# Optimization experiments

Measured on AMD Instinct MI355X. Metric: run time of the kernel, lower is better.

The kernel has to match this reference:

```python
import jax, jax.numpy as jnp
import numpy as np

N, E, F0, HEADS, B, OUT = 100000, 1600000, 128, 4, 64, 32
CHANNELS = [16, 8, 4, 2]
NEG_SLOPE = 0.2


def setup_inputs() -> dict:
    key = jax.random.key(0)
    ks = jax.random.split(key, 40)
    inp = {}
    inp['x'] = jax.random.normal(ks[0], (N, F0), dtype=jnp.float32)
    inp['edge_index'] = jax.random.randint(ks[1], (2, E), 0, N, dtype=jnp.int64)
    inp['batch'] = jnp.sort(jax.random.randint(ks[2], (N,), 0, B, dtype=jnp.int64))
    # GATConv params per layer: W [in, heads*out], att_src/att_dst [heads, out], bias [heads*out]
    in_dim = F0
    ki = 3
    for li, oc in enumerate(CHANNELS, start=1):
        scale = 1.0 / np.sqrt(in_dim)
        inp[f'W{li}'] = jax.random.normal(ks[ki], (in_dim, HEADS * oc), dtype=jnp.float32) * scale
        inp[f'a_src{li}'] = jax.random.normal(ks[ki + 1], (HEADS, oc), dtype=jnp.float32) * 0.1
        inp[f'a_dst{li}'] = jax.random.normal(ks[ki + 2], (HEADS, oc), dtype=jnp.float32) * 0.1
        inp[f'b{li}'] = jnp.zeros((HEADS * oc,), dtype=jnp.float32)
        ki += 3
        in_dim = HEADS * oc
    inp['W_fc'] = jax.random.normal(ks[ki], (2 * HEADS, OUT), dtype=jnp.float32) * (1.0 / np.sqrt(2 * HEADS))
    inp['b_fc'] = jnp.zeros((OUT,), dtype=jnp.float32)
    return inp


def gat_layer(x, src, dst, W, a_src, a_dst, b, oc):
    n = x.shape[0]
    h = (x @ W).reshape(n, HEADS, oc)                    # [N, H, C]
    al_s = jnp.einsum('nhc,hc->nh', h, a_src)            # [N, H]
    al_d = jnp.einsum('nhc,hc->nh', h, a_dst)
    e = jax.nn.leaky_relu(al_s[src] + al_d[dst], NEG_SLOPE)  # [E, H]
    # segment softmax over incoming edges per destination node
    m = jax.ops.segment_max(e, dst, num_segments=n)
    m = jnp.where(jnp.isfinite(m), m, 0.0)
    ex = jnp.exp(e - m[dst])
    s = jax.ops.segment_sum(ex, dst, num_segments=n)
    alpha = ex / (s[dst] + 1e-16)                        # [E, H]
    out = jax.ops.segment_sum(h[src] * alpha[:, :, None], dst, num_segments=n)
    return out.reshape(n, HEADS * oc) + b


def reference(x, edge_index, batch, W1, a_src1, a_dst1, b1, W2, a_src2, a_dst2, b2,
              W3, a_src3, a_dst3, b3, W4, a_src4, a_dst4, b4, W_fc, b_fc):
    n = x.shape[0]
    loops = jnp.arange(n, dtype=edge_index.dtype)
    src = jnp.concatenate([edge_index[0], loops])   # PyG GATConv adds self-loops
    dst = jnp.concatenate([edge_index[1], loops])
    params = [(W1, a_src1, a_dst1, b1), (W2, a_src2, a_dst2, b2),
              (W3, a_src3, a_dst3, b3), (W4, a_src4, a_dst4, b4)]
    h = x
    for (W, a_s, a_d, b), oc in zip(params, CHANNELS):
        h = jax.nn.relu(gat_layer(h, src, dst, W, a_s, a_d, b, oc))
        # dropout(0.3) is identity at inference
    # global mean pool over graphs in the batch
    sums = jax.ops.segment_sum(h, batch, num_segments=B)
    cnt = jax.ops.segment_sum(jnp.ones((n,), h.dtype), batch, num_segments=B)
    pooled = sums / jnp.maximum(cnt, 1.0)[:, None]
    return pooled @ W_fc + b_fc
```

## Files before the change

kernel.cpp:

```cpp
#include <hip/hip_runtime.h>
#include <hip/hip_bf16.h>

#define NNODES 100000
#define NEDGES 1600000
#define NHEADS 4
#define NGRAPH 64
#define NOUTF  32
#define BSH    9
#define NBUK   ((NNODES + 511) >> 9)
#define BPAD   16
#define BCAP   9216
#define CGRID  512
#define G1GRID ((NNODES + 63) / 64)

__device__ __forceinline__ unsigned short f2bf(float f) {
    union { float f; unsigned u; } v;
    v.f = f;
    unsigned r = v.u + 0x7FFF + ((v.u >> 16) & 1);
    return (unsigned short)(r >> 16);
}
__device__ __forceinline__ float bflo(unsigned u) {
    union { unsigned u; float f; } v;
    v.u = u << 16;
    return v.f;
}
__device__ __forceinline__ float bfhi(unsigned u) {
    union { unsigned u; float f; } v;
    v.u = u & 0xFFFF0000u;
    return v.f;
}

__device__ __forceinline__ bool ei_is_int64(const int* __restrict__ ei) {
    int acc = 0;
    #pragma unroll
    for (int i = 0; i < 32; i++) acc |= ei[2 * i + 1];
    return acc == 0;
}

__device__ __forceinline__ void fma4(float4& a, float s, const float4& b) {
    a.x += s * b.x;
    a.y += s * b.y;
    a.z += s * b.z;
    a.w += s * b.w;
}

__global__ __launch_bounds__(256) void gat_coarse_gemm1_kernel(
        const int* __restrict__ ei, const int* __restrict__ bt,
        int* __restrict__ bkcur, int* __restrict__ packed, int* __restrict__ bat,
        const float* __restrict__ x, const float* __restrict__ W1,
        const float* __restrict__ as1, const float* __restrict__ ad1,
        unsigned short* __restrict__ h1, float* __restrict__ al_s,
        float* __restrict__ al_d, int ne, int n) {
    __shared__ float smem[64 * 64 + 64 * 132];
    const int tid = threadIdx.x;
    if (blockIdx.x < CGRID) {
        int* hist = (int*)smem;
        int* base = hist + NBUK;
        for (int i = tid; i < NBUK; i += 256) hist[i] = 0;
        __syncthreads();
        bool wide = ei_is_int64(ei);
        int chunk = (ne + CGRID - 1) / CGRID;
        int e0 = blockIdx.x * chunk;
        int e1 = min(e0 + chunk, ne);
        for (int i = e0 + tid; i < e1; i += 256) {
            int d = wide ? ei[2 * (ne + i)] : ei[ne + i];
            atomicAdd(&hist[d >> BSH], 1);
        }
        __syncthreads();
        for (int i = tid; i < NBUK; i += 256)
            base[i] = hist[i] ? atomicAdd(&bkcur[i * BPAD], hist[i]) : 0;
        __syncthreads();
        for (int i = tid; i < NBUK; i += 256) hist[i] = 0;
        __syncthreads();
        for (int i = e0 + tid; i < e1; i += 256) {
            int s = wide ? ei[2 * i] : ei[i];
            int d = wide ? ei[2 * (ne + i)] : ei[ne + i];
            int bk = d >> BSH;
            int pos = base[bk] + atomicAdd(&hist[bk], 1);
            if (pos < BCAP) packed[bk * BCAP + pos] = s | ((d & 511) << 17);
        }
        int gid = blockIdx.x * 256 + tid;
        for (int i = gid; i < n; i += CGRID * 256) bat[i] = wide ? bt[2 * i] : bt[i];
    } else {
        constexpr int DIN = 128, DOUT = 64, KTILE = 64;
        constexpr int OG = DOUT / 4;
        constexpr int NPB = 64;
        constexpr int S = DIN + 4;
        constexpr int C = DOUT / NHEADS;
        float* Wl = smem;
        float* xs = smem + KTILE * DOUT;
        const int base = (blockIdx.x - CGRID) * NPB;
        constexpr int KC = DIN / 4;
        for (int i = tid; i < NPB * KC; i += 256) {
            int nn = i / KC, kc = i - nn * KC;
            int nd = base + nn;
            float4 v = (nd < n) ? ((const float4*)x)[(size_t)nd * KC + kc]
                                : make_float4(0.f, 0.f, 0.f, 0.f);
            *(float4*)&xs[nn * S + kc * 4] = v;
        }
        const int og = tid % OG;
        const int ng = tid / OG;
        const int n0 = ng * 4;
        float4 acc[4] = {};
        for (int kt = 0; kt < DIN; kt += KTILE) {
            __syncthreads();
            for (int i = tid; i < KTILE * OG; i += 256)
                ((float4*)Wl)[i] = ((const float4*)W1)[kt * OG + i];
            __syncthreads();
            #pragma unroll 2
            for (int k = 0; k < KTILE; k += 4) {
                float4 wv[4], xv[4];
                #pragma unroll
                for (int j = 0; j < 4; j++)
                    wv[j] = *(const float4*)&Wl[(k + j) * DOUT + og * 4];
                #pragma unroll
                for (int r = 0; r < 4; r++)
                    xv[r] = *(const float4*)&xs[(n0 + r) * S + kt + k];
                #pragma unroll
                for (int r = 0; r < 4; r++) {
                    fma4(acc[r], xv[r].x, wv[0]);
                    fma4(acc[r], xv[r].y, wv[1]);
                    fma4(acc[r], xv[r].z, wv[2]);
                    fma4(acc[r], xv[r].w, wv[3]);
                }
            }
        }
        float4 asv = ((const float4*)as1)[og];
        float4 adv = ((const float4*)ad1)[og];
        #pragma unroll
        for (int r = 0; r < 4; r++) {
            int node = base + n0 + r;
            bool ok = node < n;
            if (ok) {
                ushort4 o;
                o.x = f2bf(acc[r].x);
                o.y = f2bf(acc[r].y);
                o.z = f2bf(acc[r].z);
                o.w = f2bf(acc[r].w);
                ((ushort4*)h1)[(size_t)node * OG + og] = o;
            }
            float ps = acc[r].x * asv.x + acc[r].y * asv.y + acc[r].z * asv.z + acc[r].w * asv.w;
            float pd = acc[r].x * adv.x + acc[r].y * adv.y + acc[r].z * adv.z + acc[r].w * adv.w;
            #pragma unroll
            for (int off = 1; off < C / 4; off <<= 1) {
                ps += __shfl_xor(ps, off);
                pd += __shfl_xor(pd, off);
            }
            if (ok && (og % (C / 4)) == 0) {
                int hh = og / (C / 4);
                al_s[node * NHEADS + hh] = ps;
                al_d[node * NHEADS + hh] = pd;
            }
        }
    }
}

__global__ __launch_bounds__(1024) void gat_fine_kernel(
        const int* __restrict__ packed, const int* __restrict__ bkcur,
        int* __restrict__ row_ptr, int* __restrict__ col, int n) {
    __shared__ int bscan[256];
    __shared__ int dg[512];
    __shared__ int excl[512];
    __shared__ int partial[256];
    __shared__ int cur[512];
    int b = blockIdx.x;
    int tid = threadIdx.x;
    if (tid < 256) bscan[tid] = (tid < NBUK) ? bkcur[tid * BPAD] : 0;
    if (tid < 512) dg[tid] = 0;
    __syncthreads();
    for (int off = 1; off < 256; off <<= 1) {
        int u = (tid < 256 && tid >= off) ? bscan[tid - off] : 0;
        __syncthreads();
        if (tid < 256) bscan[tid] += u;
        __syncthreads();
    }
    int cntb = bkcur[b * BPAD];
    int csr0 = bscan[b] - cntb;
    int pbeg = b * BCAP;
    int pend = pbeg + cntb;
    for (int t = pbeg + tid; t < pend; t += 1024)
        atomicAdd(&dg[packed[t] >> 17], 1);
    __syncthreads();
    int a0 = 0, a1 = 0, s = 0;
    if (tid < 256) {
        a0 = dg[2 * tid];
        a1 = dg[2 * tid + 1];
        s = a0 + a1;
        partial[tid] = s;
    }
    __syncthreads();
    for (int off = 1; off < 256; off <<= 1) {
        int u = (tid < 256 && tid >= off) ? partial[tid - off] : 0;
        __syncthreads();
        if (tid < 256) partial[tid] += u;
        __syncthreads();
    }
    if (tid < 256) {
        int ebase = partial[tid] - s;
        excl[2 * tid] = ebase;
        excl[2 * tid + 1] = ebase + a0;
        cur[2 * tid] = ebase;
        cur[2 * tid + 1] = ebase + a0;
    }
    __syncthreads();
    int node0 = b << BSH;
    if (tid < 512) {
        int nd = node0 + tid;
        if (nd < n) row_ptr[nd] = csr0 + excl[tid];
    }
    if (b == NBUK - 1 && tid == 0) row_ptr[n] = bscan[NBUK - 1];
    for (int t = pbeg + tid; t < pend; t += 1024) {
        int v = packed[t];
        int pos = atomicAdd(&cur[v >> 17], 1);
        col[csr0 + pos] = v & 0x1FFFF;
    }
}

__global__ __launch_bounds__(256) void gat_agg1_gemm2_kernel(
        const unsigned short* __restrict__ h, const float* __restrict__ al_s,
        const float* __restrict__ al_d_l1, const int* __restrict__ row_ptr,
        const int* __restrict__ col, const float* __restrict__ b1,
        const float* __restrict__ W2, const float* __restrict__ as2,
        const float* __restrict__ ad2, char* __restrict__ hrow_out,
        float* __restrict__ al_d, int n) {
    __shared__ float Wl[64 * 32];
    __shared__ float xs[32 * 68];
    const int tid = threadIdx.x;
    for (int i = tid; i < 64 * 32 / 4; i += 256)
        ((float4*)Wl)[i] = ((const float4*)W2)[i];
    __syncthreads();
    int lane = tid & 63;
    int sub = lane & 7;
    int gidx = lane >> 3;
    int slot = (tid >> 6) * 8 + gidx;
    int node = blockIdx.x * 32 + slot;
    bool ok = node < n;
    int node_c = ok ? node : (n - 1);
    int beg = row_ptr[node_c];
    int cnt = row_ptr[node_c + 1] - beg;
    const uint4* h4 = (const uint4*)h;
    float acc[8] = {};
    int j0 = sub * 8;
    float ald = al_d_l1[node_c * NHEADS + sub];
    ald = al_d_l1[node_c * NHEADS + (sub >> 1)];
    const int hh = sub >> 1;
    float ws = 0.f;
    int total = cnt + 1;
    int t = 0;
    for (; t + 2 <= total; t += 2) {
        int s0 = col[beg + t];
        int s1 = (t + 1 < cnt) ? col[beg + t + 1] : node_c;
        float e0 = al_s[s0 * NHEADS + hh] + ald;
        float e1 = al_s[s1 * NHEADS + hh] + ald;
        uint4 hv0 = h4[(size_t)s0 * 8 + sub];
        uint4 hv1 = h4[(size_t)s1 * 8 + sub];
        e0 = (e0 > 0.f) ? e0 : 0.2f * e0;
        e1 = (e1 > 0.f) ? e1 : 0.2f * e1;
        float w0 = __expf(e0);
        float w1 = __expf(e1);
        ws += w0;
        acc[0] += w0 * bflo(hv0.x);
        acc[1] += w0 * bfhi(hv0.x);
        acc[2] += w0 * bflo(hv0.y);
        acc[3] += w0 * bfhi(hv0.y);
        acc[4] += w0 * bflo(hv0.z);
        acc[5] += w0 * bfhi(hv0.z);
        acc[6] += w0 * bflo(hv0.w);
        acc[7] += w0 * bfhi(hv0.w);
        ws += w1;
        acc[0] += w1 * bflo(hv1.x);
        acc[1] += w1 * bfhi(hv1.x);
        acc[2] += w1 * bflo(hv1.y);
        acc[3] += w1 * bfhi(hv1.y);
        acc[4] += w1 * bflo(hv1.z);
        acc[5] += w1 * bfhi(hv1.z);
        acc[6] += w1 * bflo(hv1.w);
        acc[7] += w1 * bfhi(hv1.w);
    }
    if (t < total) {
        int s0 = (t < cnt) ? col[beg + t] : node_c;
        float e0 = al_s[s0 * NHEADS + hh] + ald;
        uint4 hv0 = h4[(size_t)s0 * 8 + sub];
        e0 = (e0 > 0.f) ? e0 : 0.2f * e0;
        float w0 = __expf(e0);
        ws += w0;
        acc[0] += w0 * bflo(hv0.x);
        acc[1] += w0 * bfhi(hv0.x);
        acc[2] += w0 * bflo(hv0.y);
        acc[3] += w0 * bfhi(hv0.y);
        acc[4] += w0 * bflo(hv0.z);
        acc[5] += w0 * bfhi(hv0.z);
        acc[6] += w0 * bflo(hv0.w);
        acc[7] += w0 * bfhi(hv0.w);
    }
    float inv = 1.f / (ws + 1e-16f);
    #pragma unroll
    for (int k = 0; k < 8; k++) {
        acc[k] = acc[k] * inv + b1[j0 + k];
        acc[k] = (acc[k] > 0.f) ? acc[k] : 0.f;
    }
    float* xrow = &xs[slot * 68];
    *(float4*)&xrow[j0] = make_float4(acc[0], acc[1], acc[2], acc[3]);
    *(float4*)&xrow[j0 + 4] = make_float4(acc[4], acc[5], acc[6], acc[7]);
    const float4* Wl4 = (const float4*)Wl;
    float4 out4 = make_float4(0.f, 0.f, 0.f, 0.f);
    #pragma unroll 4
    for (int k = 0; k < 64; k += 4) {
        float4 xv = *(const float4*)&xrow[k];
        float4 w0 = Wl4[(k + 0) * 8 + sub];
        float4 w1 = Wl4[(k + 1) * 8 + sub];
        float4 w2 = Wl4[(k + 2) * 8 + sub];
        float4 w3 = Wl4[(k + 3) * 8 + sub];
        fma4(out4, xv.x, w0);
        fma4(out4, xv.y, w1);
        fma4(out4, xv.z, w2);
        fma4(out4, xv.w, w3);
    }
    float4 asv = ((const float4*)as2)[sub];
    float4 adv = ((const float4*)ad2)[sub];
    char* rp = hrow_out + (size_t)node_c * 96;
    if (ok) {
        ushort4 o;
        o.x = f2bf(out4.x);
        o.y = f2bf(out4.y);
        o.z = f2bf(out4.z);
        o.w = f2bf(out4.w);
        *(ushort4*)(rp + 16 + 8 * sub) = o;
    }
    float ps = out4.x * asv.x + out4.y * asv.y + out4.z * asv.z + out4.w * asv.w;
    float pd = out4.x * adv.x + out4.y * adv.y + out4.z * adv.z + out4.w * adv.w;
    ps += __shfl_xor(ps, 1);
    pd += __shfl_xor(pd, 1);
    if (ok && (sub & 1) == 0) {
        int hh2 = sub >> 1;
        *(float*)(rp + 4 * hh2) = ps;
        al_d[node_c * NHEADS + hh2] = pd;
    }
}

__global__ __launch_bounds__(256) void gat_agg2_gemm3_kernel(
        const char* __restrict__ hrow, const float* __restrict__ al_d_in,
        const int* __restrict__ row_ptr, const int* __restrict__ col,
        const float* __restrict__ b2, const float* __restrict__ W3,
        const float* __restrict__ as3, const float* __restrict__ ad3,
        char* __restrict__ hrow_out, float* __restrict__ al_d, int n) {
    __shared__ float Wl[32 * 16];
    __shared__ float xs[64 * 36];
    const int tid = threadIdx.x;
    for (int i = tid; i < 32 * 16 / 4; i += 256)
        ((float4*)Wl)[i] = ((const float4*)W3)[i];
    __syncthreads();
    int lane = tid & 63;
    int sub = lane & 3;
    int gidx = lane >> 2;
    int slot = (tid >> 6) * 16 + gidx;
    int node = blockIdx.x * 64 + slot;
    bool ok = node < n;
    int node_c = ok ? node : (n - 1);
    int beg = row_ptr[node_c];
    int cnt = row_ptr[node_c + 1] - beg;
    float acc[8] = {};
    int j0 = sub * 8;
    const int hh = sub;
    float ald = al_d_in[node_c * NHEADS + hh];
    float ws = 0.f;
    int total = cnt + 1;
    int t = 0;
    for (; t + 2 <= total; t += 2) {
        int s0 = col[beg + t];
        int s1 = (t + 1 < cnt) ? col[beg + t + 1] : node_c;
        const char* r0 = hrow + (size_t)s0 * 96;
        const char* r1 = hrow + (size_t)s1 * 96;
        float e0 = *(const float*)(r0 + 4 * hh) + ald;
        float e1 = *(const float*)(r1 + 4 * hh) + ald;
        uint4 hv0 = *(const uint4*)(r0 + 16 + 16 * sub);
        uint4 hv1 = *(const uint4*)(r1 + 16 + 16 * sub);
        e0 = (e0 > 0.f) ? e0 : 0.2f * e0;
        e1 = (e1 > 0.f) ? e1 : 0.2f * e1;
        float w0 = __expf(e0);
        float w1 = __expf(e1);
        ws += w0;
        acc[0] += w0 * bflo(hv0.x);
        acc[1] += w0 * bfhi(hv0.x);
        acc[2] += w0 * bflo(hv0.y);
        acc[3] += w0 * bfhi(hv0.y);
        acc[4] += w0 * bflo(hv0.z);
        acc[5] += w0 * bfhi(hv0.z);
        acc[6] += w0 * bflo(hv0.w);
        acc[7] += w0 * bfhi(hv0.w);
        ws += w1;
        acc[0] += w1 * bflo(hv1.x);
        acc[1] += w1 * bfhi(hv1.x);
        acc[2] += w1 * bflo(hv1.y);
        acc[3] += w1 * bfhi(hv1.y);
        acc[4] += w1 * bflo(hv1.z);
        acc[5] += w1 * bfhi(hv1.z);
        acc[6] += w1 * bflo(hv1.w);
        acc[7] += w1 * bfhi(hv1.w);
    }
    if (t < total) {
        int s0 = (t < cnt) ? col[beg + t] : node_c;
        const char* r0 = hrow + (size_t)s0 * 96;
        float e0 = *(const float*)(r0 + 4 * hh) + ald;
        uint4 hv0 = *(const uint4*)(r0 + 16 + 16 * sub);
        e0 = (e0 > 0.f) ? e0 : 0.2f * e0;
        float w0 = __expf(e0);
        ws += w0;
        acc[0] += w0 * bflo(hv0.x);
        acc[1] += w0 * bfhi(hv0.x);
        acc[2] += w0 * bflo(hv0.y);
        acc[3] += w0 * bfhi(hv0.y);
        acc[4] += w0 * bflo(hv0.z);
        acc[5] += w0 * bfhi(hv0.z);
        acc[6] += w0 * bflo(hv0.w);
        acc[7] += w0 * bfhi(hv0.w);
    }
    float inv = 1.f / (ws + 1e-16f);
    #pragma unroll
    for (int k = 0; k < 8; k++) {
        acc[k] = acc[k] * inv + b2[j0 + k];
        acc[k] = (acc[k] > 0.f) ? acc[k] : 0.f;
    }
    float* xrow = &xs[slot * 36];
    *(float4*)&xrow[j0] = make_float4(acc[0], acc[1], acc[2], acc[3]);
    *(float4*)&xrow[j0 + 4] = make_float4(acc[4], acc[5], acc[6], acc[7]);
    const float4* Wl4 = (const float4*)Wl;
    float4 out4 = make_float4(0.f, 0.f, 0.f, 0.f);
    #pragma unroll 4
    for (int k = 0; k < 32; k += 4) {
        float4 xv = *(const float4*)&xrow[k];
        float4 w0 = Wl4[(k + 0) * 4 + sub];
        float4 w1 = Wl4[(k + 1) * 4 + sub];
        float4 w2 = Wl4[(k + 2) * 4 + sub];
        float4 w3 = Wl4[(k + 3) * 4 + sub];
        fma4(out4, xv.x, w0);
        fma4(out4, xv.y, w1);
        fma4(out4, xv.z, w2);
        fma4(out4, xv.w, w3);
    }
    float4 asv = ((const float4*)as3)[sub];
    float4 adv = ((const float4*)ad3)[sub];
    char* rp = hrow_out + (size_t)node_c * 64;
    if (ok) {
        ushort4 o;
        o.x = f2bf(out4.x);
        o.y = f2bf(out4.y);
        o.z = f2bf(out4.z);
        o.w = f2bf(out4.w);
        *(ushort4*)(rp + 16 + 8 * sub) = o;
        float ps = out4.x * asv.x + out4.y * asv.y + out4.z * asv.z + out4.w * asv.w;
        float pd = out4.x * adv.x + out4.y * adv.y + out4.z * adv.z + out4.w * adv.w;
        *(float*)(rp + 4 * sub) = ps;
        al_d[node_c * NHEADS + sub] = pd;
    }
}

__global__ __launch_bounds__(256) void gat_agg3_gemm4_kernel(
        const char* __restrict__ hrow, const float* __restrict__ al_d_in,
        const int* __restrict__ row_ptr, const int* __restrict__ col,
        const float* __restrict__ b3, const float* __restrict__ W4,
        const float* __restrict__ as4, const float* __restrict__ ad4,
        char* __restrict__ hrow_out, float* __restrict__ al_d, int n) {
    __shared__ float Wl[16 * 8];
    __shared__ float xs[128 * 20];
    const int tid = threadIdx.x;
    if (tid < 16 * 8 / 4) ((float4*)Wl)[tid] = ((const float4*)W4)[tid];
    __syncthreads();
    int lane = tid & 63;
    int sub = lane & 1;
    int gidx = lane >> 1;
    int slot = (tid >> 6) * 32 + gidx;
    int node = blockIdx.x * 128 + slot;
    bool ok = node < n;
    int node_c = ok ? node : (n - 1);
    int beg = row_ptr[node_c];
    int cnt = row_ptr[node_c + 1] - beg;
    float acc[8] = {};
    int j0 = sub * 8;
    const int hh0 = 2 * sub, hh1 = 2 * sub + 1;
    float ald0 = al_d_in[node_c * NHEADS + hh0];
    float ald1 = al_d_in[node_c * NHEADS + hh1];
    float ws0 = 0.f, ws1 = 0.f;
    int total = cnt + 1;
    int t = 0;
    for (; t + 2 <= total; t += 2) {
        int s0 = col[beg + t];
        int s1 = (t + 1 < cnt) ? col[beg + t + 1] : node_c;
        const char* r0 = hrow + (size_t)s0 * 64;
        const char* r1 = hrow + (size_t)s1 * 64;
        float2 a0 = *(const float2*)(r0 + 8 * sub);
        float2 a1 = *(const float2*)(r1 + 8 * sub);
        uint4 hv0 = *(const uint4*)(r0 + 16 + 16 * sub);
        uint4 hv1 = *(const uint4*)(r1 + 16 + 16 * sub);
        float e00 = a0.x + ald0;
        float e01 = a0.y + ald1;
        float e10 = a1.x + ald0;
        float e11 = a1.y + ald1;
        e00 = (e00 > 0.f) ? e00 : 0.2f * e00;
        e01 = (e01 > 0.f) ? e01 : 0.2f * e01;
        e10 = (e10 > 0.f) ? e10 : 0.2f * e10;
        e11 = (e11 > 0.f) ? e11 : 0.2f * e11;
        float w00 = __expf(e00);
        float w01 = __expf(e01);
        float w10 = __expf(e10);
        float w11 = __expf(e11);
        ws0 += w00;
        ws1 += w01;
        acc[0] += w00 * bflo(hv0.x);
        acc[1] += w00 * bfhi(hv0.x);
        acc[2] += w00 * bflo(hv0.y);
        acc[3] += w00 * bfhi(hv0.y);
        acc[4] += w01 * bflo(hv0.z);
        acc[5] += w01 * bfhi(hv0.z);
        acc[6] += w01 * bflo(hv0.w);
        acc[7] += w01 * bfhi(hv0.w);
        ws0 += w10;
        ws1 += w11;
        acc[0] += w10 * bflo(hv1.x);
        acc[1] += w10 * bfhi(hv1.x);
        acc[2] += w10 * bflo(hv1.y);
        acc[3] += w10 * bfhi(hv1.y);
        acc[4] += w11 * bflo(hv1.z);
        acc[5] += w11 * bfhi(hv1.z);
        acc[6] += w11 * bflo(hv1.w);
        acc[7] += w11 * bfhi(hv1.w);
    }
    if (t < total) {
        int s0 = (t < cnt) ? col[beg + t] : node_c;
        const char* r0 = hrow + (size_t)s0 * 64;
        float2 a0 = *(const float2*)(r0 + 8 * sub);
        uint4 hv0 = *(const uint4*)(r0 + 16 + 16 * sub);
        float e00 = a0.x + ald0;
        float e01 = a0.y + ald1;
        e00 = (e00 > 0.f) ? e00 : 0.2f * e00;
        e01 = (e01 > 0.f) ? e01 : 0.2f * e01;
        float w00 = __expf(e00);
        float w01 = __expf(e01);
        ws0 += w00;
        ws1 += w01;
        acc[0] += w00 * bflo(hv0.x);
        acc[1] += w00 * bfhi(hv0.x);
        acc[2] += w00 * bflo(hv0.y);
        acc[3] += w00 * bfhi(hv0.y);
        acc[4] += w01 * bflo(hv0.z);
        acc[5] += w01 * bfhi(hv0.z);
        acc[6] += w01 * bflo(hv0.w);
        acc[7] += w01 * bfhi(hv0.w);
    }
    float inv0 = 1.f / (ws0 + 1e-16f);
    float inv1 = 1.f / (ws1 + 1e-16f);
    #pragma unroll
    for (int k = 0; k < 4; k++) {
        acc[k] = acc[k] * inv0 + b3[j0 + k];
        acc[k] = (acc[k] > 0.f) ? acc[k] : 0.f;
    }
    #pragma unroll
    for (int k = 4; k < 8; k++) {
        acc[k] = acc[k] * inv1 + b3[j0 + k];
        acc[k] = (acc[k] > 0.f) ? acc[k] : 0.f;
    }
    float* xrow = &xs[slot * 20];
    *(float4*)&xrow[j0] = make_float4(acc[0], acc[1], acc[2], acc[3]);
    *(float4*)&xrow[j0 + 4] = make_float4(acc[4], acc[5], acc[6], acc[7]);
    const float4* Wl4 = (const float4*)Wl;
    float4 out4 = make_float4(0.f, 0.f, 0.f, 0.f);
    #pragma unroll
    for (int k = 0; k < 16; k += 4) {
        float4 xv = *(const float4*)&xrow[k];
        float4 w0 = Wl4[(k + 0) * 2 + sub];
        float4 w1 = Wl4[(k + 1) * 2 + sub];
        float4 w2 = Wl4[(k + 2) * 2 + sub];
        float4 w3 = Wl4[(k + 3) * 2 + sub];
        fma4(out4, xv.x, w0);
        fma4(out4, xv.y, w1);
        fma4(out4, xv.z, w2);
        fma4(out4, xv.w, w3);
    }
    float4 asv = ((const float4*)as4)[sub];
    float4 adv = ((const float4*)ad4)[sub];
    char* rp = hrow_out + (size_t)node_c * 64;
    if (ok) {
        *(float4*)(rp + 16 + 16 * sub) = out4;
        *(float*)(rp + 8 * sub)     = out4.x * asv.x + out4.y * asv.y;
        *(float*)(rp + 8 * sub + 4) = out4.z * asv.z + out4.w * asv.w;
        al_d[node_c * NHEADS + 2 * sub]     = out4.x * adv.x + out4.y * adv.y;
        al_d[node_c * NHEADS + 2 * sub + 1] = out4.z * adv.z + out4.w * adv.w;
    }
}

__global__ __launch_bounds__(256) void gat_agg_f32row_kernel(
        const char* __restrict__ hrow, const float* __restrict__ al_d,
        const int* __restrict__ row_ptr, const int* __restrict__ col,
        const float* __restrict__ bias, float* __restrict__ out, int n) {
    constexpr int L = 2;
    constexpr int PW = 32;
    int lane = threadIdx.x & 63;
    int sub = lane & 1;
    int gidx = lane >> 1;
    int node = blockIdx.x * (4 * PW) + (threadIdx.x >> 6) * PW + gidx;
    if (node >= n) return;
    int beg = row_ptr[node];
    int cnt = row_ptr[node + 1] - beg;
    const int hh0 = 2 * sub, hh1 = 2 * sub + 1;
    float ald0 = al_d[node * NHEADS + hh0];
    float ald1 = al_d[node * NHEADS + hh1];
    float4 acc = make_float4(0.f, 0.f, 0.f, 0.f);
    float ws0 = 0.f, ws1 = 0.f;
    int total = cnt + 1;
    int t = 0;
    for (; t + 2 <= total; t += 2) {
        int s0 = col[beg + t];
        int s1 = (t + 1 < cnt) ? col[beg + t + 1] : node;
        const char* r0 = hrow + (size_t)s0 * 64;
        const char* r1 = hrow + (size_t)s1 * 64;
        float2 a0 = *(const float2*)(r0 + 8 * sub);
        float2 a1 = *(const float2*)(r1 + 8 * sub);
        float4 hv0 = *(const float4*)(r0 + 16 + 16 * sub);
        float4 hv1 = *(const float4*)(r1 + 16 + 16 * sub);
        float e00 = a0.x + ald0;
        float e01 = a0.y + ald1;
        float e10 = a1.x + ald0;
        float e11 = a1.y + ald1;
        e00 = (e00 > 0.f) ? e00 : 0.2f * e00;
        e01 = (e01 > 0.f) ? e01 : 0.2f * e01;
        e10 = (e10 > 0.f) ? e10 : 0.2f * e10;
        e11 = (e11 > 0.f) ? e11 : 0.2f * e11;
        float w00 = __expf(e00);
        float w01 = __expf(e01);
        float w10 = __expf(e10);
        float w11 = __expf(e11);
        ws0 += w00;
        ws1 += w01;
        acc.x += w00 * hv0.x;
        acc.y += w00 * hv0.y;
        acc.z += w01 * hv0.z;
        acc.w += w01 * hv0.w;
        ws0 += w10;
        ws1 += w11;
        acc.x += w10 * hv1.x;
        acc.y += w10 * hv1.y;
        acc.z += w11 * hv1.z;
        acc.w += w11 * hv1.w;
    }
    if (t < total) {
        int s0 = (t < cnt) ? col[beg + t] : node;
        const char* r0 = hrow + (size_t)s0 * 64;
        float2 a0 = *(const float2*)(r0 + 8 * sub);
        float4 hv0 = *(const float4*)(r0 + 16 + 16 * sub);
        float e00 = a0.x + ald0;
        float e01 = a0.y + ald1;
        e00 = (e00 > 0.f) ? e00 : 0.2f * e00;
        e01 = (e01 > 0.f) ? e01 : 0.2f * e01;
        float w00 = __expf(e00);
        float w01 = __expf(e01);
        ws0 += w00;
        ws1 += w01;
        acc.x += w00 * hv0.x;
        acc.y += w00 * hv0.y;
        acc.z += w01 * hv0.z;
        acc.w += w01 * hv0.w;
    }
    float4 bv = ((const float4*)bias)[sub];
    float4 v;
    v.x = acc.x / (ws0 + 1e-16f) + bv.x;
    v.y = acc.y / (ws0 + 1e-16f) + bv.y;
    v.z = acc.z / (ws1 + 1e-16f) + bv.z;
    v.w = acc.w / (ws1 + 1e-16f) + bv.w;
    v.x = (v.x > 0.f) ? v.x : 0.f;
    v.y = (v.y > 0.f) ? v.y : 0.f;
    v.z = (v.z > 0.f) ? v.z : 0.f;
    v.w = (v.w > 0.f) ? v.w : 0.f;
    ((float4*)out)[(size_t)node * L + sub] = v;
}

__global__ __launch_bounds__(256) void gat_poolfc_kernel(
        const float* __restrict__ x, const int* __restrict__ bat,
        const float* __restrict__ Wfc, const float* __restrict__ bfc,
        float* __restrict__ out, int n) {
    __shared__ float sh[256][9];
    int b = blockIdx.x;
    int tid = threadIdx.x;
    int lo = 0, hi = n;
    while (lo < hi) { int mid = (lo + hi) >> 1; if (bat[mid] < b) lo = mid + 1; else hi = mid; }
    int i0 = lo;
    hi = n;
    while (lo < hi) { int mid = (lo + hi) >> 1; if (bat[mid] < b + 1) lo = mid + 1; else hi = mid; }
    int i1 = lo;
    float a[8] = {};
    for (int i = i0 + tid; i < i1; i += 256) {
        float4 v0 = ((const float4*)x)[(size_t)i * 2];
        float4 v1 = ((const float4*)x)[(size_t)i * 2 + 1];
        a[0] += v0.x; a[1] += v0.y; a[2] += v0.z; a[3] += v0.w;
        a[4] += v1.x; a[5] += v1.y; a[6] += v1.z; a[7] += v1.w;
    }
    #pragma unroll
    for (int k = 0; k < 8; k++) sh[tid][k] = a[k];
    __syncthreads();
    for (int off = 128; off >= 1; off >>= 1) {
        if (tid < off)
            #pragma unroll
            for (int k = 0; k < 8; k++) sh[tid][k] += sh[tid + off][k];
        __syncthreads();
    }
    if (tid < NOUTF) {
        float c = (float)(i1 - i0);
        if (c < 1.f) c = 1.f;
        float acc = bfc[tid];
        #pragma unroll
        for (int d = 0; d < 8; d++) acc += (sh[0][d] / c) * Wfc[d * NOUTF + tid];
        out[b * NOUTF + tid] = acc;
    }
}

extern "C" void kernel_launch(void* const* d_in, const int* in_sizes, int n_in,
                              void* d_out, int out_size, void* d_ws, size_t ws_size,
                              hipStream_t stream) {
    const float* x = (const float*)d_in[0];
    const int* ei = (const int*)d_in[1];
    const int* batch = (const int*)d_in[2];
    const float* W1 = (const float*)d_in[3];
    const float* as1 = (const float*)d_in[4];
    const float* ad1 = (const float*)d_in[5];
    const float* b1 = (const float*)d_in[6];
    const float* W2 = (const float*)d_in[7];
    const float* as2 = (const float*)d_in[8];
    const float* ad2 = (const float*)d_in[9];
    const float* b2 = (const float*)d_in[10];
    const float* W3 = (const float*)d_in[11];
    const float* as3 = (const float*)d_in[12];
    const float* ad3 = (const float*)d_in[13];
    const float* b3 = (const float*)d_in[14];
    const float* W4 = (const float*)d_in[15];
    const float* as4 = (const float*)d_in[16];
    const float* ad4 = (const float*)d_in[17];
    const float* b4 = (const float*)d_in[18];
    const float* Wfc = (const float*)d_in[19];
    const float* bfc = (const float*)d_in[20];

    const int n = NNODES, ne = NEDGES;

    char* p = (char*)d_ws;
    auto carve = [&](size_t bytes) {
        char* r = p;
        p += (bytes + 255) & ~(size_t)255;
        return r;
    };
    int* row_ptr = (int*)carve((size_t)(n + 1) * 4);
    int* col = (int*)carve((size_t)ne * 4);
    int* bkcur = (int*)carve(256 * BPAD * 4);
    int* packed = (int*)carve((size_t)NBUK * BCAP * 4);
    float* buf_h = (float*)carve((size_t)n * 64 * 4);
    float* buf_x = (float*)carve((size_t)n * 64 * 4);
    float* al_s = (float*)carve((size_t)n * NHEADS * 4);
    float* al_d = (float*)carve((size_t)n * NHEADS * 4);
    int* bat = (int*)carve((size_t)n * 4);
    unsigned short* h_bf16 = (unsigned short*)buf_h;

    hipMemsetAsync(bkcur, 0, 256 * BPAD * 4, stream);

    gat_coarse_gemm1_kernel<<<CGRID + G1GRID, 256, 0, stream>>>(
        ei, batch, bkcur, packed, bat, x, W1, as1, ad1, h_bf16, al_s, al_d, ne, n);

    gat_fine_kernel<<<NBUK, 1024, 0, stream>>>(packed, bkcur, row_ptr, col, n);

    gat_agg1_gemm2_kernel<<<(n + 31) / 32, 256, 0, stream>>>(
        h_bf16, al_s, al_d, row_ptr, col, b1, W2, as2, ad2, (char*)buf_x, al_d, n);

    gat_agg2_gemm3_kernel<<<(n + 63) / 64, 256, 0, stream>>>(
        (const char*)buf_x, al_d, row_ptr, col, b2, W3, as3, ad3, (char*)buf_h, al_d, n);

    gat_agg3_gemm4_kernel<<<(n + 127) / 128, 256, 0, stream>>>(
        (const char*)buf_h, al_d, row_ptr, col, b3, W4, as4, ad4, (char*)buf_x, al_d, n);

    gat_agg_f32row_kernel<<<(n + 127) / 128, 256, 0, stream>>>(
        (const char*)buf_x, al_d, row_ptr, col, b4, buf_h, n);

    gat_poolfc_kernel<<<NGRAPH, 256, 0, stream>>>(buf_h, bat, Wfc, bfc, (float*)d_out, n);
}
```

Baseline: 345.0 us.

## Fuse final aggregation with mean-pool atomics and stage edges in LDS

The last GAT aggregation now accumulates its per-node ReLU outputs straight into per-graph sums. It does this with shared-memory atomics for up to four graphs per block and global atomics otherwise, so the layer-4 output array never has to be written and then re-read by a separate pool kernel. The FC kernel becomes a small per-graph epilogue that reads these sums. The coarse bucketing pass caches each block's src/dst edge chunk in shared memory so the second pass does not reload edge_index from global memory. It also removes a redundant al_d load. Float atomics make the pooled sums order-nondeterministic, and an extra memset is added.

```diff
diff --git a/kernel.cpp b/kernel.cpp
--- a/kernel.cpp
+++ b/kernel.cpp
@@ -11,6 +11,7 @@
 #define BPAD   16
 #define BCAP   9216
 #define CGRID  512
+#define ECAP   ((NEDGES + CGRID - 1) / CGRID)
 #define G1GRID ((NNODES + 63) / 64)
 
 __device__ __forceinline__ unsigned short f2bf(float f) {
@@ -55,7 +56,9 @@
     const int tid = threadIdx.x;
     if (blockIdx.x < CGRID) {
         int* hist = (int*)smem;
-        int* base = hist + NBUK;
+        int* base = hist + 256;
+        int* es = base + 256;
+        int* ed = es + ECAP;
         for (int i = tid; i < NBUK; i += 256) hist[i] = 0;
         __syncthreads();
         bool wide = ei_is_int64(ei);
@@ -63,7 +66,10 @@
         int e0 = blockIdx.x * chunk;
         int e1 = min(e0 + chunk, ne);
         for (int i = e0 + tid; i < e1; i += 256) {
+            int s = wide ? ei[2 * i] : ei[i];
             int d = wide ? ei[2 * (ne + i)] : ei[ne + i];
+            es[i - e0] = s;
+            ed[i - e0] = d;
             atomicAdd(&hist[d >> BSH], 1);
         }
         __syncthreads();
@@ -72,12 +78,12 @@
         __syncthreads();
         for (int i = tid; i < NBUK; i += 256) hist[i] = 0;
         __syncthreads();
-        for (int i = e0 + tid; i < e1; i += 256) {
-            int s = wide ? ei[2 * i] : ei[i];
-            int d = wide ? ei[2 * (ne + i)] : ei[ne + i];
+        int m = e1 - e0;
+        for (int j = tid; j < m; j += 256) {
+            int d = ed[j];
             int bk = d >> BSH;
             int pos = base[bk] + atomicAdd(&hist[bk], 1);
-            if (pos < BCAP) packed[bk * BCAP + pos] = s | ((d & 511) << 17);
+            if (pos < BCAP) packed[bk * BCAP + pos] = es[j] | ((d & 511) << 17);
         }
         int gid = blockIdx.x * 256 + tid;
         for (int i = gid; i < n; i += CGRID * 256) bat[i] = wide ? bt[2 * i] : bt[i];
@@ -241,9 +247,8 @@
     const uint4* h4 = (const uint4*)h;
     float acc[8] = {};
     int j0 = sub * 8;
-    float ald = al_d_l1[node_c * NHEADS + sub];
-    ald = al_d_l1[node_c * NHEADS + (sub >> 1)];
     const int hh = sub >> 1;
+    float ald = al_d_l1[node_c * NHEADS + hh];
     float ws = 0.f;
     int total = cnt + 1;
     int t = 0;
@@ -588,29 +593,39 @@
     }
 }
 
-__global__ __launch_bounds__(256) void gat_agg_f32row_kernel(
+__global__ __launch_bounds__(256) void gat_agg4_pool_kernel(
         const char* __restrict__ hrow, const float* __restrict__ al_d,
         const int* __restrict__ row_ptr, const int* __restrict__ col,
-        const float* __restrict__ bias, float* __restrict__ out, int n) {
-    constexpr int L = 2;
-    constexpr int PW = 32;
-    int lane = threadIdx.x & 63;
+        const float* __restrict__ bias, const int* __restrict__ bat,
+        float* __restrict__ sums, int n) {
+    __shared__ float gsum[4 * 8];
+    __shared__ int g0s;
+    const int tid = threadIdx.x;
+    if (tid < 32) gsum[tid] = 0.f;
+    if (tid == 0) {
+        int fn = blockIdx.x * 128;
+        g0s = bat[fn < n ? fn : (n - 1)];
+    }
+    __syncthreads();
+    int g0 = g0s;
+    int lane = tid & 63;
     int sub = lane & 1;
     int gidx = lane >> 1;
-    int node = blockIdx.x * (4 * PW) + (threadIdx.x >> 6) * PW + gidx;
-    if (node >= n) return;
-    int beg = row_ptr[node];
-    int cnt = row_ptr[node + 1] - beg;
+    int node = blockIdx.x * 128 + (tid >> 6) * 32 + gidx;
+    bool ok = node < n;
+    int node_c = ok ? node : (n - 1);
+    int beg = row_ptr[node_c];
+    int cnt = row_ptr[node_c + 1] - beg;
     const int hh0 = 2 * sub, hh1 = 2 * sub + 1;
-    float ald0 = al_d[node * NHEADS + hh0];
-    float ald1 = al_d[node * NHEADS + hh1];
+    float ald0 = al_d[node_c * NHEADS + hh0];
+    float ald1 = al_d[node_c * NHEADS + hh1];
     float4 acc = make_float4(0.f, 0.f, 0.f, 0.f);
     float ws0 = 0.f, ws1 = 0.f;
     int total = cnt + 1;
     int t = 0;
     for (; t + 2 <= total; t += 2) {
         int s0 = col[beg + t];
-        int s1 = (t + 1 < cnt) ? col[beg + t + 1] : node;
+        int s1 = (t + 1 < cnt) ? col[beg + t + 1] : node_c;
         const char* r0 = hrow + (size_t)s0 * 64;
         const char* r1 = hrow + (size_t)s1 * 64;
         float2 a0 = *(const float2*)(r0 + 8 * sub);
@@ -643,7 +658,7 @@
         acc.w += w11 * hv1.w;
     }
     if (t < total) {
-        int s0 = (t < cnt) ? col[beg + t] : node;
+        int s0 = (t < cnt) ? col[beg + t] : node_c;
         const char* r0 = hrow + (size_t)s0 * 64;
         float2 a0 = *(const float2*)(r0 + 8 * sub);
         float4 hv0 = *(const float4*)(r0 + 16 + 16 * sub);
@@ -670,14 +685,33 @@
     v.y = (v.y > 0.f) ? v.y : 0.f;
     v.z = (v.z > 0.f) ? v.z : 0.f;
     v.w = (v.w > 0.f) ? v.w : 0.f;
-    ((float4*)out)[(size_t)node * L + sub] = v;
-}
-
-__global__ __launch_bounds__(256) void gat_poolfc_kernel(
-        const float* __restrict__ x, const int* __restrict__ bat,
+    if (ok) {
+        int g = bat[node];
+        int dg = g - g0;
+        if (dg < 4) {
+            atomicAdd(&gsum[dg * 8 + 4 * sub + 0], v.x);
+            atomicAdd(&gsum[dg * 8 + 4 * sub + 1], v.y);
+            atomicAdd(&gsum[dg * 8 + 4 * sub + 2], v.z);
+            atomicAdd(&gsum[dg * 8 + 4 * sub + 3], v.w);
+        } else {
+            atomicAdd(&sums[g * 8 + 4 * sub + 0], v.x);
+            atomicAdd(&sums[g * 8 + 4 * sub + 1], v.y);
+            atomicAdd(&sums[g * 8 + 4 * sub + 2], v.z);
+            atomicAdd(&sums[g * 8 + 4 * sub + 3], v.w);
+        }
+    }
+    __syncthreads();
+    if (tid < 32) {
+        int dg = tid >> 3, k = tid & 7;
+        int g = g0 + dg;
+        if (g < NGRAPH) atomicAdd(&sums[g * 8 + k], gsum[tid]);
+    }
+}
+
+__global__ __launch_bounds__(64) void gat_fc_kernel(
+        const float* __restrict__ sums, const int* __restrict__ bat,
         const float* __restrict__ Wfc, const float* __restrict__ bfc,
         float* __restrict__ out, int n) {
-    __shared__ float sh[256][9];
     int b = blockIdx.x;
     int tid = threadIdx.x;
     int lo = 0, hi = n;
@@ -686,28 +720,12 @@
     hi = n;
     while (lo < hi) { int mid = (lo + hi) >> 1; if (bat[mid] < b + 1) lo = mid + 1; else hi = mid; }
     int i1 = lo;
-    float a[8] = {};
-    for (int i = i0 + tid; i < i1; i += 256) {
-        float4 v0 = ((const float4*)x)[(size_t)i * 2];
-        float4 v1 = ((const float4*)x)[(size_t)i * 2 + 1];
-        a[0] += v0.x; a[1] += v0.y; a[2] += v0.z; a[3] += v0.w;
-        a[4] += v1.x; a[5] += v1.y; a[6] += v1.z; a[7] += v1.w;
-    }
-    #pragma unroll
-    for (int k = 0; k < 8; k++) sh[tid][k] = a[k];
-    __syncthreads();
-    for (int off = 128; off >= 1; off >>= 1) {
-        if (tid < off)
-            #pragma unroll
-            for (int k = 0; k < 8; k++) sh[tid][k] += sh[tid + off][k];
-        __syncthreads();
-    }
     if (tid < NOUTF) {
         float c = (float)(i1 - i0);
         if (c < 1.f) c = 1.f;
         float acc = bfc[tid];
         #pragma unroll
-        for (int d = 0; d < 8; d++) acc += (sh[0][d] / c) * Wfc[d * NOUTF + tid];
+        for (int d = 0; d < 8; d++) acc += (sums[b * 8 + d] / c) * Wfc[d * NOUTF + tid];
         out[b * NOUTF + tid] = acc;
     }
 }
@@ -754,9 +772,11 @@
     float* al_s = (float*)carve((size_t)n * NHEADS * 4);
     float* al_d = (float*)carve((size_t)n * NHEADS * 4);
     int* bat = (int*)carve((size_t)n * 4);
+    float* sums = (float*)carve((size_t)NGRAPH * 8 * 4);
     unsigned short* h_bf16 = (unsigned short*)buf_h;
 
     hipMemsetAsync(bkcur, 0, 256 * BPAD * 4, stream);
+    hipMemsetAsync(sums, 0, NGRAPH * 8 * 4, stream);
 
     gat_coarse_gemm1_kernel<<<CGRID + G1GRID, 256, 0, stream>>>(
         ei, batch, bkcur, packed, bat, x, W1, as1, ad1, h_bf16, al_s, al_d, ne, n);
@@ -772,8 +792,8 @@
     gat_agg3_gemm4_kernel<<<(n + 127) / 128, 256, 0, stream>>>(
         (const char*)buf_h, al_d, row_ptr, col, b3, W4, as4, ad4, (char*)buf_x, al_d, n);
 
-    gat_agg_f32row_kernel<<<(n + 127) / 128, 256, 0, stream>>>(
-        (const char*)buf_x, al_d, row_ptr, col, b4, buf_h, n);
-
-    gat_poolfc_kernel<<<NGRAPH, 256, 0, stream>>>(buf_h, bat, Wfc, bfc, (float*)d_out, n);
-}
+    gat_agg4_pool_kernel<<<(n + 127) / 128, 256, 0, stream>>>(
+        (const char*)buf_x, al_d, row_ptr, col, b4, bat, sums, n);
+
+    gat_fc_kernel<<<NGRAPH, 64, 0, stream>>>(sums, bat, Wfc, bfc, (float*)d_out, n);
+}
```

After: 342.9 us (median of 2 runs). Within noise of the previous version (-0.6%).
